# Performance work log

Measured on AMD Instinct MI355X. Metric: run time of the kernel, lower is better.

## Reference

```python
import jax, jax.numpy as jnp
import numpy as np

B, T, U = 4, 300, 100
D_E, D_P, D_MODEL, VOCAB = 512, 512, 512, 1024


def setup_inputs() -> dict:
    key = jax.random.key(0)
    ks = jax.random.split(key, 8)
    s = lambda d: 1.0 / np.sqrt(d)
    return {
        "encoder_outputs": jax.random.normal(ks[0], (B, T, D_E), jnp.float32),
        "predictor_outputs": jax.random.normal(ks[1], (B, U, D_P), jnp.float32),
        "W_enc": jax.random.normal(ks[2], (D_E, D_MODEL), jnp.float32) * s(D_E),
        "b_enc": jnp.zeros((D_MODEL,), jnp.float32),
        "W_pred": jax.random.normal(ks[3], (D_P, D_MODEL), jnp.float32) * s(D_P),
        "b_pred": jnp.zeros((D_MODEL,), jnp.float32),
        "W_joint": jax.random.normal(ks[4], (D_MODEL, VOCAB), jnp.float32) * s(D_MODEL),
        "b_joint": jnp.zeros((VOCAB,), jnp.float32),
    }


def reference(encoder_outputs, predictor_outputs, W_enc, b_enc, W_pred, b_pred, W_joint, b_joint):
    # f: [B, T, D], g: [B, U, D]
    f = jnp.einsum("bte,ed->btd", encoder_outputs, W_enc) + b_enc
    g = jnp.einsum("bup,pd->bud", predictor_outputs, W_pred) + b_pred
    # broadcast add -> [B, T, U, D], tanh activation
    joint_inputs = jnp.tanh(f[:, :, None, :] + g[:, None, :, :])
    # vocab projection -> [B, T, U, V]
    joint_outs = jnp.einsum("btud,dv->btuv", joint_inputs, W_joint) + b_joint
    return joint_outs
```

## Files before the change

### kernel.cpp

```cpp
#include <hip/hip_runtime.h>
#include <hip/hip_bf16.h>
#include <cstdint>


typedef __attribute__((ext_vector_type(4))) float f32x4;
typedef __attribute__((ext_vector_type(8))) short s16x8;

#define B_ 4
#define T_ 300
#define U_ 100
#define DM 512
#define VOC 1024
#define M_MAIN (B_*T_*U_)
#define M_ENC_PAD 1280
#define M_PRED_PAD 512

__device__ __forceinline__ unsigned short f2bf(float x) {
  unsigned int u = __builtin_bit_cast(unsigned int, x);
  u += 0x7FFFu + ((u >> 16) & 1u);
  return (unsigned short)(u >> 16);
}

__device__ __forceinline__ float fast_tanh(float x) {
  float e = __builtin_amdgcn_exp2f(x * 2.8853900817779268f);
  return fmaf(-2.0f, __builtin_amdgcn_rcpf(e + 1.0f), 1.0f);
}

__device__ __forceinline__ void gload_lds16(const void* g, void* l) {
  __builtin_amdgcn_global_load_lds(
      (const __attribute__((address_space(1))) void*)g,
      (__attribute__((address_space(3))) void*)l, 16, 0, 0);
}

__global__ void k_cvtpad(const float* __restrict__ enc, const float* __restrict__ pred,
                         unsigned short* __restrict__ encb, unsigned short* __restrict__ predb)
{
  int idx = blockIdx.x * 256 + threadIdx.x;
  const int encCh = M_ENC_PAD * 64;
  const float* src; unsigned short* dst; int Mv; int id2;
  if (idx < encCh) { src = enc; dst = encb; Mv = B_*T_; id2 = idx; }
  else            { id2 = idx - encCh; src = pred; dst = predb; Mv = B_*U_; }
  int r = id2 >> 6, k = (id2 & 63) * 8;
  s16x8 v;
  if (r < Mv) {
    f32x4 a = *(const f32x4*)(src + r*DM + k);
    f32x4 b = *(const f32x4*)(src + r*DM + k + 4);
#pragma unroll
    for (int j = 0; j < 4; ++j) { v[j] = (short)f2bf(a[j]); v[4+j] = (short)f2bf(b[j]); }
  } else {
#pragma unroll
    for (int j = 0; j < 8; ++j) v[j] = 0;
  }
  *(s16x8*)(dst + (long)id2 * 8) = v;
}

__global__ void k_transpose3(const float* __restrict__ We, const float* __restrict__ Wp,
                             const float* __restrict__ Wj,
                             unsigned short* __restrict__ WeT, unsigned short* __restrict__ WpT,
                             unsigned short* __restrict__ WjT)
{
  __shared__ float tile[32][33];
  const float* src; unsigned short* dst; int Ccols;
  const int R = 512;
  if (blockIdx.z == 0)      { src = We; dst = WeT; Ccols = 512; }
  else if (blockIdx.z == 1) { src = Wp; dst = WpT; Ccols = 512; }
  else                      { src = Wj; dst = WjT; Ccols = 1024; }
  int bx = blockIdx.x, by = blockIdx.y;
  if (bx * 32 >= Ccols) return;
  int x = threadIdx.x & 31, y = threadIdx.x >> 5;
  int c0 = bx * 32, r0 = by * 32;
#pragma unroll
  for (int i = 0; i < 4; ++i)
    tile[y + i*8][x] = src[(r0 + y + i*8) * Ccols + c0 + x];
  __syncthreads();
#pragma unroll
  for (int i = 0; i < 4; ++i)
    dst[(c0 + y + i*8) * R + r0 + x] = f2bf(tile[x][y + i*8]);
}

__device__ __forceinline__ void gemm_body(const unsigned short* __restrict__ A,
                                          const unsigned short* __restrict__ Bt,
                                          const float* __restrict__ bias,
                                          float* __restrict__ C,
                                          int Mvalid, int ldc, int mt, int nt)
{
  __shared__ unsigned short lza[128*64];
  __shared__ unsigned short lzb[128*64];
  const int tid  = threadIdx.x;
  const int wave = tid >> 6;
  const int lane = tid & 63;
  const int row0 = mt * 128;
  const int col0 = nt * 128;
  const int wm = (wave >> 1) * 64;
  const int wn = (wave & 1) * 64;

  const int rloc0 = wave*32 + (lane >> 3);
  const int srcc  = (lane & 7) ^ (rloc0 & 7);
  const unsigned short* gA = A  + (row0 + rloc0)*DM + srcc*8;
  const unsigned short* gB = Bt + (col0 + rloc0)*DM + srcc*8;
  unsigned short* ldsA = &lza[(wave*32)*64];
  unsigned short* ldsB = &lzb[(wave*32)*64];

  f32x4 acc[4][4] = {};

  for (int kt = 0; kt < DM/64; ++kt) {
    __syncthreads();
#pragma unroll
    for (int i = 0; i < 4; ++i) {
      gload_lds16(gA + i*8*DM, ldsA + i*8*64);
      gload_lds16(gB + i*8*DM, ldsB + i*8*64);
    }
    gA += 64; gB += 64;
    __syncthreads();
#pragma unroll
    for (int kk = 0; kk < 2; ++kk) {
      s16x8 af[4], bfr[4];
#pragma unroll
      for (int m = 0; m < 4; ++m) {
        int r = wm + m*16 + (lane & 15);
        int c = (kk*4 + (lane >> 4)) ^ (r & 7);
        af[m] = *(const s16x8*)&lza[r*64 + c*8];
      }
#pragma unroll
      for (int n = 0; n < 4; ++n) {
        int r = wn + n*16 + (lane & 15);
        int c = (kk*4 + (lane >> 4)) ^ (r & 7);
        bfr[n] = *(const s16x8*)&lzb[r*64 + c*8];
      }
#pragma unroll
      for (int m = 0; m < 4; ++m)
#pragma unroll
        for (int n = 0; n < 4; ++n)
          acc[m][n] = __builtin_amdgcn_mfma_f32_16x16x32_bf16(af[m], bfr[n], acc[m][n], 0, 0, 0);
    }
  }

  const int cl = lane & 15, rq = (lane >> 4) * 4;
#pragma unroll
  for (int n = 0; n < 4; ++n) {
    int col = col0 + wn + n*16 + cl;
    float bv = bias[col];
#pragma unroll
    for (int m = 0; m < 4; ++m) {
      int rb = row0 + wm + m*16 + rq;
#pragma unroll
      for (int j = 0; j < 4; ++j) {
        int r = rb + j;
        if (r < Mvalid) __builtin_nontemporal_store(acc[m][n][j] + bv, &C[(long)r * ldc + col]);
      }
    }
  }
}

__global__ __launch_bounds__(256, 2) void k_gemm_fg(
    const unsigned short* __restrict__ encb,  const unsigned short* __restrict__ WeT,
    const float* __restrict__ b_enc,  float* __restrict__ f,
    const unsigned short* __restrict__ predb, const unsigned short* __restrict__ WpT,
    const float* __restrict__ b_pred, float* __restrict__ g)
{
  const unsigned short* A;  const unsigned short* Bt;
  const float* bias; float* C; int Mv;
  if (blockIdx.z == 0) { A = encb;  Bt = WeT; bias = b_enc;  C = f; Mv = M_ENC_PAD; }
  else {
    if (blockIdx.x >= M_PRED_PAD/128) return;
    A = predb; Bt = WpT; bias = b_pred; C = g; Mv = M_PRED_PAD;
  }
  gemm_body(A, Bt, bias, C, Mv, DM, blockIdx.x, blockIdx.y);
}

__global__ __launch_bounds__(512, 4) void k_joint_fused(
    const float* __restrict__ f, const float* __restrict__ g,
    const unsigned short* __restrict__ Bt, const float* __restrict__ bias,
    float* __restrict__ C)
{
  __shared__ unsigned short lds[24576];

  const int bid = blockIdx.x;
  const int mt = bid >> 2, nt = bid & 3;
  const int row0 = mt * 128;
  const int t = threadIdx.x, w = t >> 6, l = t & 63;
  const int wm = w >> 2, wn = w & 3, lr = l & 15, lc = l >> 4;

  int arow = row0 + (t >> 2); if (arow >= M_MAIN) arow = M_MAIN - 1;
  int bb  = arow / (T_*U_);
  int rem = arow - bb * (T_*U_);
  int tt  = rem / U_;
  int uu  = rem - tt * U_;
  const float* fp = f + (bb*T_ + tt) * DM + (t & 3) * 8;
  const float* gp = g + (bb*U_ + uu) * DM + (t & 3) * 8;
  const int awr = (t >> 2)*32 + (((t & 3) + ((t >> 2) >> 1)) & 3)*8;

  const unsigned short* gBs[2];
#pragma unroll
  for (int i = 0; i < 2; ++i) {
    int ch = (i*8 + w)*64 + l;
    int br = ch >> 2;
    int cg = ((ch & 3) - ((ch >> 3) & 3)) & 3;
    gBs[i] = Bt + (long)(nt*256 + br) * DM + cg*8;
  }

  int offA[4], offB[4];
#pragma unroll
  for (int m = 0; m < 4; ++m) {
    int r = wm*64 + m*16 + lr;
    offA[m] = r*32 + ((lc + (r >> 1)) & 3)*8;
  }
#pragma unroll
  for (int n = 0; n < 4; ++n) {
    int r = wn*64 + n*16 + lr;
    offB[n] = r*32 + ((lc + (r >> 1)) & 3)*8;
  }

  f32x4 acc[4][4] = {};

  {
#pragma unroll
    for (int i = 0; i < 2; ++i)
      gload_lds16(gBs[i], &lds[8192 + (i*8 + w)*512]);
    f32x4 fa0 = *(const f32x4*)(fp);
    f32x4 fa1 = *(const f32x4*)(fp + 4);
    f32x4 ga0 = *(const f32x4*)(gp);
    f32x4 ga1 = *(const f32x4*)(gp + 4);
    s16x8 v;
#pragma unroll
    for (int j = 0; j < 4; ++j) {
      v[j]   = (short)f2bf(fast_tanh(fa0[j] + ga0[j]));
      v[4+j] = (short)f2bf(fast_tanh(fa1[j] + ga1[j]));
    }
    *(s16x8*)&lds[awr] = v;
  }
  __syncthreads();

#pragma unroll
  for (int kt = 0; kt < 16; ++kt) {
    const int cur = kt & 1, nxt = cur ^ 1;

    if (kt < 15) {
#pragma unroll
      for (int i = 0; i < 2; ++i)
        gload_lds16(gBs[i] + (kt+1)*32, &lds[8192 + nxt*8192 + (i*8 + w)*512]);
      {
        const float* fpk = fp + (kt+1)*32;
        const float* gpk = gp + (kt+1)*32;
        f32x4 fa0 = *(const f32x4*)(fpk);
        f32x4 fa1 = *(const f32x4*)(fpk + 4);
        f32x4 ga0 = *(const f32x4*)(gpk);
        f32x4 ga1 = *(const f32x4*)(gpk + 4);
        s16x8 v;
#pragma unroll
        for (int j = 0; j < 4; ++j) {
          v[j]   = (short)f2bf(fast_tanh(fa0[j] + ga0[j]));
          v[4+j] = (short)f2bf(fast_tanh(fa1[j] + ga1[j]));
        }
        *(s16x8*)&lds[nxt*4096 + awr] = v;
      }
    }

    s16x8 af[4], bfv[4];
#pragma unroll
    for (int m = 0; m < 4; ++m) af[m] = *(const s16x8*)&lds[cur*4096 + offA[m]];
#pragma unroll
    for (int n = 0; n < 4; ++n) bfv[n] = *(const s16x8*)&lds[8192 + cur*8192 + offB[n]];

    __builtin_amdgcn_s_setprio(1);
#pragma unroll
    for (int m = 0; m < 4; ++m)
#pragma unroll
      for (int n = 0; n < 4; ++n)
        acc[m][n] = __builtin_amdgcn_mfma_f32_16x16x32_bf16(af[m], bfv[n], acc[m][n], 0, 0, 0);
    __builtin_amdgcn_s_setprio(0);

    __syncthreads();
  }

  const int rq = lc * 4;
#pragma unroll
  for (int n = 0; n < 4; ++n) {
    int col = nt*256 + wn*64 + n*16 + lr;
    float bv = bias[col];
#pragma unroll
    for (int m = 0; m < 4; ++m) {
      int rb = row0 + wm*64 + m*16 + rq;
#pragma unroll
      for (int j = 0; j < 4; ++j) {
        int r = rb + j;
        if (r < M_MAIN)
          __builtin_nontemporal_store(acc[m][n][j] + bv, &C[(long)r * VOC + col]);
      }
    }
  }
}

extern "C" void kernel_launch(void* const* d_in, const int* in_sizes, int n_in,
                              void* d_out, int out_size, void* d_ws, size_t ws_size,
                              hipStream_t stream)
{
  const float* enc    = (const float*)d_in[0];
  const float* pred   = (const float*)d_in[1];
  const float* W_enc  = (const float*)d_in[2];
  const float* b_enc  = (const float*)d_in[3];
  const float* W_pred = (const float*)d_in[4];
  const float* b_pred = (const float*)d_in[5];
  const float* W_joint= (const float*)d_in[6];
  const float* b_joint= (const float*)d_in[7];
  float* out = (float*)d_out;

  char* w = (char*)d_ws;
  unsigned short* encb  = (unsigned short*)w; w += (long)M_ENC_PAD*DM*2;
  unsigned short* predb = (unsigned short*)w; w += (long)M_PRED_PAD*DM*2;
  unsigned short* WeT   = (unsigned short*)w; w += (long)DM*DM*2;
  unsigned short* WpT   = (unsigned short*)w; w += (long)DM*DM*2;
  unsigned short* WjT   = (unsigned short*)w; w += (long)VOC*DM*2;
  float*          f     = (float*)w;          w += (long)M_ENC_PAD*DM*4;
  float*          g     = (float*)w;          w += (long)M_PRED_PAD*DM*4;

  k_cvtpad     <<<dim3(448),       dim3(256), 0, stream>>>(enc, pred, encb, predb);
  k_transpose3 <<<dim3(32, 16, 3), dim3(256), 0, stream>>>(W_enc, W_pred, W_joint, WeT, WpT, WjT);
  k_gemm_fg    <<<dim3(10, 4, 2),  dim3(256), 0, stream>>>(encb, WeT, b_enc, f, predb, WpT, b_pred, g);
  k_joint_fused<<<dim3(938*4),     dim3(512), 0, stream>>>(f, g, WjT, b_joint, out);
}
```

Measured before the change: 316.4 us.

## Stage f/g tiles into LDS asynchronously and tile joint GEMM per batch

The joint kernel now uses a 3D grid (vocab tile, row block, batch) so each block's rows stay inside one batch. For each K slice it copies the block's 100 g rows and a few f rows into swizzled LDS buffers with async global-to-LDS loads, prefetched two steps ahead, then builds the tanh/bf16 A tile from LDS. Previously each thread read f and g from global memory directly, with repeated uncoalesced reads. The change uses far more LDS (about 74KB per block), which may reduce occupancy against the launch bound of 4, and it adds a deeper pipeline.

Result: faster. 295.7 us (-6.5%).

```diff
diff --git a/kernel.cpp b/kernel.cpp
--- a/kernel.cpp
+++ b/kernel.cpp
@@ -173,94 +173,97 @@
     const unsigned short* __restrict__ Bt, const float* __restrict__ bias,
     float* __restrict__ C)
 {
-  __shared__ unsigned short lds[24576];
-
-  const int bid = blockIdx.x;
-  const int mt = bid >> 2, nt = bid & 3;
-  const int row0 = mt * 128;
+  __shared__ char smem[75776];
+
+  const int nt = blockIdx.x;
+  const int jb = blockIdx.y;
+  const int b  = blockIdx.z;
   const int t = threadIdx.x, w = t >> 6, l = t & 63;
   const int wm = w >> 2, wn = w & 3, lr = l & 15, lc = l >> 4;
 
-  int arow = row0 + (t >> 2); if (arow >= M_MAIN) arow = M_MAIN - 1;
-  int bb  = arow / (T_*U_);
-  int rem = arow - bb * (T_*U_);
-  int tt  = rem / U_;
-  int uu  = rem - tt * U_;
-  const float* fp = f + (bb*T_ + tt) * DM + (t & 3) * 8;
-  const float* gp = g + (bb*U_ + uu) * DM + (t & 3) * 8;
-  const int awr = (t >> 2)*32 + (((t & 3) + ((t >> 2) >> 1)) & 3)*8;
-
-  const unsigned short* gBs[2];
-#pragma unroll
-  for (int i = 0; i < 2; ++i) {
-    int ch = (i*8 + w)*64 + l;
+  const int i = t >> 2, c = t & 3;
+  int lcl = jb*128 + i; if (lcl > T_*U_ - 1) lcl = T_*U_ - 1;
+  const int u  = lcl % U_;
+  const int tl = lcl / U_;
+  const int bt0l = (jb*128) / U_;
+  const int jf = tl - bt0l;
+  const int goff0 = u*128 + (((2*c    ) + u) & 7)*16;
+  const int goff1 = u*128 + (((2*c + 1) + u) & 7)*16;
+  const int foff0 = jf*128 + (((2*c    ) + jf) & 7)*16;
+  const int foff1 = jf*128 + (((2*c + 1) + jf) & 7)*16;
+  const int awr   = i*64 + ((c + (i >> 1)) & 3)*16;
+
+  const unsigned short* gBs[2]; int Bdst[2];
+#pragma unroll
+  for (int s = 0; s < 2; ++s) {
+    int ch = (s*8 + w)*64 + l;
     int br = ch >> 2;
     int cg = ((ch & 3) - ((ch >> 3) & 3)) & 3;
-    gBs[i] = Bt + (long)(nt*256 + br) * DM + cg*8;
-  }
+    gBs[s] = Bt + (long)(nt*256 + br) * DM + cg*8;
+    Bdst[s] = (s*8 + w)*1024;
+  }
+  const int chA = w*64 + l;
+  const float* gsrcA = g + (long)(b*U_ + (chA >> 3)) * DM + (((chA & 7) - (chA >> 3)) & 7)*4;
+  const int gdstA = w*1024;
+  const int chB2 = 512 + w*64 + l;
+  const float* gsrcB = g + (long)(b*U_ + (chB2 >> 3)) * DM + (((chB2 & 7) - (chB2 >> 3)) & 7)*4;
+  const int gdstB = 8192 + w*1024;
+  const bool isF = (t >= 448 && t < 480);
+  int frow = bt0l + (l >> 3); if (frow > T_ - 1) frow = T_ - 1;
+  const float* fsrc = f + (long)(b*T_ + frow) * DM + (((l & 7) - (l >> 3)) & 7)*4;
 
   int offA[4], offB[4];
 #pragma unroll
   for (int m = 0; m < 4; ++m) {
     int r = wm*64 + m*16 + lr;
-    offA[m] = r*32 + ((lc + (r >> 1)) & 3)*8;
+    offA[m] = r*64 + ((lc + (r >> 1)) & 3)*16;
   }
 #pragma unroll
   for (int n = 0; n < 4; ++n) {
     int r = wn*64 + n*16 + lr;
-    offB[n] = r*32 + ((lc + (r >> 1)) & 3)*8;
-  }
+    offB[n] = r*64 + ((lc + (r >> 1)) & 3)*16;
+  }
+
+#define STAGE_B(kt_, v_) { \
+    gload_lds16(gBs[0] + (kt_)*32, smem + 16384 + (v_)*16384 + Bdst[0]); \
+    gload_lds16(gBs[1] + (kt_)*32, smem + 16384 + (v_)*16384 + Bdst[1]); }
+#define STAGE_GF(kt_, v_) { \
+    gload_lds16(gsrcA + (kt_)*32, smem + 49152 + (v_)*12800 + gdstA); \
+    if (t < 288) gload_lds16(gsrcB + (kt_)*32, smem + 49152 + (v_)*12800 + gdstB); \
+    if (isF)     gload_lds16(fsrc  + (kt_)*32, smem + 74752 + (v_)*512); }
+#define BUILD_A(v_) { \
+    f32x4 ga0 = *(const f32x4*)(smem + 49152 + (v_)*12800 + goff0); \
+    f32x4 ga1 = *(const f32x4*)(smem + 49152 + (v_)*12800 + goff1); \
+    f32x4 fa0 = *(const f32x4*)(smem + 74752 + (v_)*512 + foff0); \
+    f32x4 fa1 = *(const f32x4*)(smem + 74752 + (v_)*512 + foff1); \
+    s16x8 v; \
+    _Pragma("unroll") \
+    for (int jj = 0; jj < 4; ++jj) { \
+      v[jj]   = (short)f2bf(fast_tanh(fa0[jj] + ga0[jj])); \
+      v[4+jj] = (short)f2bf(fast_tanh(fa1[jj] + ga1[jj])); \
+    } \
+    *(s16x8*)(smem + (v_)*8192 + awr) = v; }
 
   f32x4 acc[4][4] = {};
 
-  {
-#pragma unroll
-    for (int i = 0; i < 2; ++i)
-      gload_lds16(gBs[i], &lds[8192 + (i*8 + w)*512]);
-    f32x4 fa0 = *(const f32x4*)(fp);
-    f32x4 fa1 = *(const f32x4*)(fp + 4);
-    f32x4 ga0 = *(const f32x4*)(gp);
-    f32x4 ga1 = *(const f32x4*)(gp + 4);
-    s16x8 v;
-#pragma unroll
-    for (int j = 0; j < 4; ++j) {
-      v[j]   = (short)f2bf(fast_tanh(fa0[j] + ga0[j]));
-      v[4+j] = (short)f2bf(fast_tanh(fa1[j] + ga1[j]));
-    }
-    *(s16x8*)&lds[awr] = v;
-  }
+  STAGE_B(0, 0); STAGE_GF(0, 0);
+  __syncthreads();
+  STAGE_GF(1, 1);
+  BUILD_A(0);
   __syncthreads();
 
 #pragma unroll
   for (int kt = 0; kt < 16; ++kt) {
     const int cur = kt & 1, nxt = cur ^ 1;
-
-    if (kt < 15) {
-#pragma unroll
-      for (int i = 0; i < 2; ++i)
-        gload_lds16(gBs[i] + (kt+1)*32, &lds[8192 + nxt*8192 + (i*8 + w)*512]);
-      {
-        const float* fpk = fp + (kt+1)*32;
-        const float* gpk = gp + (kt+1)*32;
-        f32x4 fa0 = *(const f32x4*)(fpk);
-        f32x4 fa1 = *(const f32x4*)(fpk + 4);
-        f32x4 ga0 = *(const f32x4*)(gpk);
-        f32x4 ga1 = *(const f32x4*)(gpk + 4);
-        s16x8 v;
-#pragma unroll
-        for (int j = 0; j < 4; ++j) {
-          v[j]   = (short)f2bf(fast_tanh(fa0[j] + ga0[j]));
-          v[4+j] = (short)f2bf(fast_tanh(fa1[j] + ga1[j]));
-        }
-        *(s16x8*)&lds[nxt*4096 + awr] = v;
-      }
-    }
+    if (kt < 15) STAGE_B(kt + 1, nxt);
+    if (kt < 14) STAGE_GF(kt + 2, cur);
+    if (kt < 15) BUILD_A(nxt);
 
     s16x8 af[4], bfv[4];
 #pragma unroll
-    for (int m = 0; m < 4; ++m) af[m] = *(const s16x8*)&lds[cur*4096 + offA[m]];
-#pragma unroll
-    for (int n = 0; n < 4; ++n) bfv[n] = *(const s16x8*)&lds[8192 + cur*8192 + offB[n]];
+    for (int m = 0; m < 4; ++m) af[m] = *(const s16x8*)(smem + cur*8192 + offA[m]);
+#pragma unroll
+    for (int n = 0; n < 4; ++n) bfv[n] = *(const s16x8*)(smem + 16384 + cur*16384 + offB[n]);
 
     __builtin_amdgcn_s_setprio(1);
 #pragma unroll
@@ -270,7 +273,7 @@
         acc[m][n] = __builtin_amdgcn_mfma_f32_16x16x32_bf16(af[m], bfv[n], acc[m][n], 0, 0, 0);
     __builtin_amdgcn_s_setprio(0);
 
-    __syncthreads();
+    if (kt < 15) __syncthreads();
   }
 
   const int rq = lc * 4;
@@ -280,15 +283,19 @@
     float bv = bias[col];
 #pragma unroll
     for (int m = 0; m < 4; ++m) {
-      int rb = row0 + wm*64 + m*16 + rq;
-#pragma unroll
-      for (int j = 0; j < 4; ++j) {
-        int r = rb + j;
-        if (r < M_MAIN)
-          __builtin_nontemporal_store(acc[m][n][j] + bv, &C[(long)r * VOC + col]);
+      int rl = jb*128 + wm*64 + m*16 + rq;
+#pragma unroll
+      for (int j2 = 0; j2 < 4; ++j2) {
+        int rowl = rl + j2;
+        if (rowl < T_*U_)
+          __builtin_nontemporal_store(acc[m][n][j2] + bv,
+                                      &C[(long)(b*(T_*U_) + rowl) * VOC + col]);
       }
     }
   }
+#undef STAGE_B
+#undef STAGE_GF
+#undef BUILD_A
 }
 
 extern "C" void kernel_launch(void* const* d_in, const int* in_sizes, int n_in,
@@ -317,5 +324,5 @@
   k_cvtpad     <<<dim3(448),       dim3(256), 0, stream>>>(enc, pred, encb, predb);
   k_transpose3 <<<dim3(32, 16, 3), dim3(256), 0, stream>>>(W_enc, W_pred, W_joint, WeT, WpT, WjT);
   k_gemm_fg    <<<dim3(10, 4, 2),  dim3(256), 0, stream>>>(encb, WeT, b_enc, f, predb, WpT, b_pred, g);
-  k_joint_fused<<<dim3(938*4),     dim3(512), 0, stream>>>(f, g, WjT, b_joint, out);
-}
+  k_joint_fused<<<dim3(4, 235, 4), dim3(512), 0, stream>>>(f, g, WjT, b_joint, out);
+}
```
